# Optimization experiments

Hardware: AMD Instinct MI355X
Metric: run time of the kernel (lower is better)

Reference implementation:

```python
import jax, jax.numpy as jnp
import numpy as np

HIDDEN = 512
BATCH = 32
SEQ = 4096


def setup_inputs() -> dict:
    key = jax.random.key(0)
    ks = jax.random.split(key, 8)
    s = 1.0 / np.sqrt(HIDDEN)
    return {
        "encoder_outputs": jax.random.normal(ks[0], (BATCH, SEQ, HIDDEN), jnp.float32),
        "decoder_hidden": jax.random.normal(ks[1], (BATCH, HIDDEN), jnp.float32),
        "W_enc": jax.random.uniform(ks[2], (HIDDEN, HIDDEN), jnp.float32, -s, s),
        "b_enc": jax.random.uniform(ks[3], (HIDDEN,), jnp.float32, -s, s),
        "W_dec": jax.random.uniform(ks[4], (HIDDEN, HIDDEN), jnp.float32, -s, s),
        "b_dec": jax.random.uniform(ks[5], (HIDDEN,), jnp.float32, -s, s),
        "W_v": jax.random.uniform(ks[6], (HIDDEN, 1), jnp.float32, -s, s),
        "b_v": jax.random.uniform(ks[7], (1,), jnp.float32, -s, s),
    }


def reference(encoder_outputs, decoder_hidden, W_enc, b_enc, W_dec, b_dec, W_v, b_v):
    # (b, s, h) projected encoder states
    enc_proj = jnp.einsum("bsh,hk->bsk", encoder_outputs, W_enc) + b_enc
    # (b, 1, h) projected decoder state, broadcast-added over seq
    dec_proj = (decoder_hidden @ W_dec + b_dec)[:, None, :]
    # score: (b, s, 1)
    score = jnp.tanh(enc_proj + dec_proj) @ W_v + b_v
    attention_weights = jax.nn.softmax(score, axis=1)  # softmax over seq_len
    # context: (b, h) weighted sum of encoder outputs
    context = jnp.sum(attention_weights * encoder_outputs, axis=1)
    return context, jnp.squeeze(attention_weights, -1)
```

## Files before the change

### kernel.cpp

```cpp
#include <hip/hip_runtime.h>
#include <hip/hip_bf16.h>

typedef __attribute__((ext_vector_type(8))) short bf16x8;
typedef __attribute__((ext_vector_type(4))) float f32x4;

#define HID 512
#define NB 32
#define SEQL 4096
#define BM 64
#define NBLK 2048

#define WS_BP    0
#define WS_DPROJ (512*1024)
#define WS_SUM   (576*1024)

__device__ __forceinline__ short f2bf(float f) {
    unsigned u = __float_as_uint(f);
    unsigned r = (u + 0x7fffu + ((u >> 16) & 1u)) >> 16;
    return (short)r;
}

__device__ __forceinline__ float fast_tanh(float x) {
    float e = __expf(2.0f * x);
    float r = __builtin_amdgcn_rcpf(e + 1.0f);
    return 1.0f - 2.0f * r;
}

__global__ void k_pre(const float* __restrict__ We, short* __restrict__ Bp,
                      const float* __restrict__ dec, const float* __restrict__ Wd,
                      const float* __restrict__ be, const float* __restrict__ bd,
                      float* __restrict__ dproj, float* __restrict__ out,
                      float* __restrict__ sumacc) {
    const int blk = blockIdx.x, t = threadIdx.x;
    if (blk < 128) {
        int tid  = blk * 256 + t;
        int lane = tid & 63;
        int nt   = (tid >> 6) & 31;
        int kc   = tid >> 11;
        int k0   = kc * 32 + (lane >> 4) * 8;
        int n    = nt * 16 + (lane & 15);
        bf16x8 v;
#pragma unroll
        for (int j = 0; j < 8; ++j) v[j] = f2bf(We[(size_t)(k0 + j) * HID + n]);
        *(bf16x8*)&Bp[(size_t)tid * 8] = v;
    } else if (blk < 640) {
        __shared__ float red[8][33];
        int bid2 = blk - 128;
        int b  = bid2 >> 4, kg = bid2 & 15;
        int kl = t & 31,    hc = t >> 5;
        int k  = kg * 32 + kl;
        const float* dr = dec + (size_t)b * HID;
        float a = 0.f;
#pragma unroll 8
        for (int j = 0; j < 64; ++j) {
            int h = hc * 64 + j;
            a += dr[h] * Wd[(size_t)h * HID + k];
        }
        red[hc][kl] = a;
        __syncthreads();
        if (hc == 0) {
            float s = be[k] + bd[k];
#pragma unroll
            for (int c = 0; c < 8; ++c) s += red[c][kl];
            dproj[(size_t)b * HID + k] = s;
        }
    } else {
        int bz = blk - 640;
        out[bz * 256 + t] = 0.f;
        if (bz == 0 && t < NB) sumacc[t] = 0.f;
    }
}

__global__ __launch_bounds__(256, 2)
void k_main(const float* __restrict__ E, const short* __restrict__ Bp,
            const float* __restrict__ dproj, const float* __restrict__ Wv,
            float* __restrict__ out, float* __restrict__ sumacc) {
    __shared__ short As[2][BM][40];
    __shared__ float fbuf[640];
    __shared__ float pbuf[BM];

    const int tid  = threadIdx.x;
    const int wave = tid >> 6, lane = tid & 63;
    const int quad = lane >> 4, l15 = lane & 15;
    const int bid  = blockIdx.x;
    const int row0 = bid * BM;
    const int b    = bid >> 6;

    f32x4 acc[4][8];
#pragma unroll
    for (int r = 0; r < 4; ++r)
#pragma unroll
        for (int c = 0; c < 8; ++c) acc[r][c] = (f32x4){0.f, 0.f, 0.f, 0.f};

    const int arow = tid >> 2, ac8 = (tid & 3) * 8;
    const float* aptr = E + (size_t)(row0 + arow) * HID + ac8;

    const short* bpw = Bp + ((size_t)(wave * 8) * 64 + lane) * 8;

    {
        float4 a0 = *(const float4*)(aptr);
        float4 a1 = *(const float4*)(aptr + 4);
        bf16x8 av;
        av[0] = f2bf(a0.x); av[1] = f2bf(a0.y); av[2] = f2bf(a0.z); av[3] = f2bf(a0.w);
        av[4] = f2bf(a1.x); av[5] = f2bf(a1.y); av[6] = f2bf(a1.z); av[7] = f2bf(a1.w);
        *(bf16x8*)&As[0][arow][ac8] = av;
        __syncthreads();
    }

    for (int kc = 0; kc < 16; ++kc) {
        const int cur = kc & 1, nxt = cur ^ 1;
        float4 a0, a1;
        if (kc < 15) {
            a0 = *(const float4*)(aptr + (kc + 1) * 32);
            a1 = *(const float4*)(aptr + (kc + 1) * 32 + 4);
        }
        bf16x8 fa[4];
#pragma unroll
        for (int r = 0; r < 4; ++r)
            fa[r] = *(bf16x8*)&As[cur][r * 16 + l15][quad * 8];
        const short* bsrc = bpw + (size_t)kc * 16384;
        bf16x8 fb[8];
#pragma unroll
        for (int c = 0; c < 8; ++c)
            fb[c] = *(const bf16x8*)(bsrc + c * 512);
#pragma unroll
        for (int c = 0; c < 8; ++c)
#pragma unroll
            for (int r = 0; r < 4; ++r)
                acc[r][c] = __builtin_amdgcn_mfma_f32_16x16x32_bf16(fa[r], fb[c], acc[r][c], 0, 0, 0);
        if (kc < 15) {
            bf16x8 av;
            av[0] = f2bf(a0.x); av[1] = f2bf(a0.y); av[2] = f2bf(a0.z); av[3] = f2bf(a0.w);
            av[4] = f2bf(a1.x); av[5] = f2bf(a1.y); av[6] = f2bf(a1.z); av[7] = f2bf(a1.w);
            *(bf16x8*)&As[nxt][arow][ac8] = av;
        }
        __syncthreads();
    }

    float part[4][4];
#pragma unroll
    for (int r = 0; r < 4; ++r)
#pragma unroll
        for (int g = 0; g < 4; ++g) part[r][g] = 0.f;
    const float* dp = dproj + (size_t)b * HID;
#pragma unroll
    for (int c = 0; c < 8; ++c) {
        int col = wave * 128 + c * 16 + l15;
        float dv = dp[col];
        float wv = Wv[col];
#pragma unroll
        for (int r = 0; r < 4; ++r)
#pragma unroll
            for (int g = 0; g < 4; ++g)
                part[r][g] += fast_tanh(acc[r][c][g] + dv) * wv;
    }
#pragma unroll
    for (int r = 0; r < 4; ++r)
#pragma unroll
        for (int g = 0; g < 4; ++g) {
            float v = part[r][g];
            v += __shfl_xor(v, 1); v += __shfl_xor(v, 2);
            v += __shfl_xor(v, 4); v += __shfl_xor(v, 8);
            part[r][g] = v;
        }
    if (l15 == 0) {
#pragma unroll
        for (int r = 0; r < 4; ++r)
#pragma unroll
            for (int g = 0; g < 4; ++g)
                fbuf[wave * 64 + r * 16 + quad * 4 + g] = part[r][g];
    }
    __syncthreads();
    if (tid < 64) {
        float s  = fbuf[tid] + fbuf[64 + tid] + fbuf[128 + tid] + fbuf[192 + tid];
        float pv = __expf(s);
        pbuf[tid] = pv;
        out[(size_t)NB * HID + row0 + tid] = pv;
        float t2 = pv;
        t2 += __shfl_xor(t2, 1);  t2 += __shfl_xor(t2, 2);  t2 += __shfl_xor(t2, 4);
        t2 += __shfl_xor(t2, 8);  t2 += __shfl_xor(t2, 16); t2 += __shfl_xor(t2, 32);
        if (tid == 0) atomicAdd(&sumacc[b], t2);
    }
    __syncthreads();

    const int hq = tid & 127, rh = tid >> 7;
    const float4* E4 = (const float4*)E;
    size_t cbase = (size_t)(row0 + rh * 32) * (HID / 4) + hq;
    float4 ca = {0.f, 0.f, 0.f, 0.f};
#pragma unroll 4
    for (int rr = 0; rr < 32; ++rr) {
        float w  = pbuf[rh * 32 + rr];
        float4 e = E4[cbase + (size_t)rr * (HID / 4)];
        ca.x += w * e.x; ca.y += w * e.y; ca.z += w * e.z; ca.w += w * e.w;
    }
    if (rh == 1) {
        fbuf[hq] = ca.x; fbuf[128 + hq] = ca.y; fbuf[256 + hq] = ca.z; fbuf[384 + hq] = ca.w;
    }
    __syncthreads();
    if (rh == 0) {
        ca.x += fbuf[hq]; ca.y += fbuf[128 + hq]; ca.z += fbuf[256 + hq]; ca.w += fbuf[384 + hq];
        float* cg = out + (size_t)b * HID + hq * 4;
        atomicAdd(cg + 0, ca.x); atomicAdd(cg + 1, ca.y);
        atomicAdd(cg + 2, ca.z); atomicAdd(cg + 3, ca.w);
    }
}

__global__ void k_finish(float* __restrict__ out, const float* __restrict__ sumacc) {
    int idx = blockIdx.x * 256 + threadIdx.x;
    if (idx < NB * HID) {
        out[idx] *= 1.0f / sumacc[idx >> 9];
    } else {
        int w = idx - NB * HID;
        out[idx] *= 1.0f / sumacc[w >> 12];
    }
}

extern "C" void kernel_launch(void* const* d_in, const int* in_sizes, int n_in,
                              void* d_out, int out_size, void* d_ws, size_t ws_size,
                              hipStream_t stream) {
    const float* E   = (const float*)d_in[0];
    const float* dec = (const float*)d_in[1];
    const float* We  = (const float*)d_in[2];
    const float* be  = (const float*)d_in[3];
    const float* Wd  = (const float*)d_in[4];
    const float* bd  = (const float*)d_in[5];
    const float* Wv  = (const float*)d_in[6];
    float* out = (float*)d_out;
    char*  ws  = (char*)d_ws;
    short* Bp     = (short*)(ws + WS_BP);
    float* dproj  = (float*)(ws + WS_DPROJ);
    float* sumacc = (float*)(ws + WS_SUM);

    k_pre<<<704, 256, 0, stream>>>(We, Bp, dec, Wd, be, bd, dproj, out, sumacc);
    k_main<<<NBLK, 256, 0, stream>>>(E, Bp, dproj, Wv, out, sumacc);
    k_finish<<<576, 256, 0, stream>>>(out, sumacc);
}
```

Measured before the change: 513.1 us.

## Drop LDS staging for A, halve row tile, stagger K start per block

Each wave now loads its A fragments straight from global memory into registers and converts them with packed bf16 conversion instructions, so the LDS double buffer and the per-iteration barriers are gone. The row tile shrinks from 64 to 32 so the grid doubles, and occupancy is raised to 3 blocks per SIMD. The K-chunk start is rotated per block to spread contention on the shared B matrix. In exchange every wave re-reads the same A rows from global memory (redundant loads across the four waves), the launch count doubles, and there are twice as many context atomics.

```diff
diff --git a/kernel.cpp b/kernel.cpp
--- a/kernel.cpp
+++ b/kernel.cpp
@@ -7,8 +7,8 @@
 #define HID 512
 #define NB 32
 #define SEQL 4096
-#define BM 64
-#define NBLK 2048
+#define BM 32
+#define NBLK 4096
 
 #define WS_BP    0
 #define WS_DPROJ (512*1024)
@@ -24,6 +24,18 @@
     float e = __expf(2.0f * x);
     float r = __builtin_amdgcn_rcpf(e + 1.0f);
     return 1.0f - 2.0f * r;
+}
+
+__device__ __forceinline__ unsigned cvtpk(float lo, float hi) {
+    unsigned r;
+    asm("v_cvt_pk_bf16_f32 %0, %1, %2" : "=v"(r) : "v"(lo), "v"(hi));
+    return r;
+}
+__device__ __forceinline__ bf16x8 pack8(const float4& A, const float4& B) {
+    union { unsigned u[4]; bf16x8 v; } t;
+    t.u[0] = cvtpk(A.x, A.y); t.u[1] = cvtpk(A.z, A.w);
+    t.u[2] = cvtpk(B.x, B.y); t.u[3] = cvtpk(B.z, B.w);
+    return t.v;
 }
 
 __global__ void k_pre(const float* __restrict__ We, short* __restrict__ Bp,
@@ -71,12 +83,11 @@
     }
 }
 
-__global__ __launch_bounds__(256, 2)
+__global__ __launch_bounds__(256, 3)
 void k_main(const float* __restrict__ E, const short* __restrict__ Bp,
             const float* __restrict__ dproj, const float* __restrict__ Wv,
             float* __restrict__ out, float* __restrict__ sumacc) {
-    __shared__ short As[2][BM][40];
-    __shared__ float fbuf[640];
+    __shared__ float fbuf[512];
     __shared__ float pbuf[BM];
 
     const int tid  = threadIdx.x;
@@ -84,62 +95,53 @@
     const int quad = lane >> 4, l15 = lane & 15;
     const int bid  = blockIdx.x;
     const int row0 = bid * BM;
-    const int b    = bid >> 6;
-
-    f32x4 acc[4][8];
-#pragma unroll
-    for (int r = 0; r < 4; ++r)
+    const int b    = bid >> 7;
+    const int stag = bid & 15;
+
+    f32x4 acc[2][8];
+#pragma unroll
+    for (int r = 0; r < 2; ++r)
 #pragma unroll
         for (int c = 0; c < 8; ++c) acc[r][c] = (f32x4){0.f, 0.f, 0.f, 0.f};
 
-    const int arow = tid >> 2, ac8 = (tid & 3) * 8;
-    const float* aptr = E + (size_t)(row0 + arow) * HID + ac8;
-
+    const float* a0p = E + (size_t)(row0 + l15) * HID + quad * 8;
+    const float* a1p = E + (size_t)(row0 + 16 + l15) * HID + quad * 8;
     const short* bpw = Bp + ((size_t)(wave * 8) * 64 + lane) * 8;
 
-    {
-        float4 a0 = *(const float4*)(aptr);
-        float4 a1 = *(const float4*)(aptr + 4);
-        bf16x8 av;
-        av[0] = f2bf(a0.x); av[1] = f2bf(a0.y); av[2] = f2bf(a0.z); av[3] = f2bf(a0.w);
-        av[4] = f2bf(a1.x); av[5] = f2bf(a1.y); av[6] = f2bf(a1.z); av[7] = f2bf(a1.w);
-        *(bf16x8*)&As[0][arow][ac8] = av;
-        __syncthreads();
-    }
+    int kcs = stag;
+    float4 a00 = *(const float4*)(a0p + kcs * 32);
+    float4 a01 = *(const float4*)(a0p + kcs * 32 + 4);
+    float4 a10 = *(const float4*)(a1p + kcs * 32);
+    float4 a11 = *(const float4*)(a1p + kcs * 32 + 4);
 
     for (int kc = 0; kc < 16; ++kc) {
-        const int cur = kc & 1, nxt = cur ^ 1;
-        float4 a0, a1;
-        if (kc < 15) {
-            a0 = *(const float4*)(aptr + (kc + 1) * 32);
-            a1 = *(const float4*)(aptr + (kc + 1) * 32 + 4);
-        }
-        bf16x8 fa[4];
-#pragma unroll
-        for (int r = 0; r < 4; ++r)
-            fa[r] = *(bf16x8*)&As[cur][r * 16 + l15][quad * 8];
-        const short* bsrc = bpw + (size_t)kc * 16384;
+        const short* bsrc = bpw + (size_t)kcs * 16384;
         bf16x8 fb[8];
 #pragma unroll
         for (int c = 0; c < 8; ++c)
             fb[c] = *(const bf16x8*)(bsrc + c * 512);
-#pragma unroll
-        for (int c = 0; c < 8; ++c)
-#pragma unroll
-            for (int r = 0; r < 4; ++r)
-                acc[r][c] = __builtin_amdgcn_mfma_f32_16x16x32_bf16(fa[r], fb[c], acc[r][c], 0, 0, 0);
+        const int kn = (kcs + 1) & 15;
+        float4 n00, n01, n10, n11;
         if (kc < 15) {
-            bf16x8 av;
-            av[0] = f2bf(a0.x); av[1] = f2bf(a0.y); av[2] = f2bf(a0.z); av[3] = f2bf(a0.w);
-            av[4] = f2bf(a1.x); av[5] = f2bf(a1.y); av[6] = f2bf(a1.z); av[7] = f2bf(a1.w);
-            *(bf16x8*)&As[nxt][arow][ac8] = av;
-        }
-        __syncthreads();
-    }
-
-    float part[4][4];
-#pragma unroll
-    for (int r = 0; r < 4; ++r)
+            n00 = *(const float4*)(a0p + kn * 32);
+            n01 = *(const float4*)(a0p + kn * 32 + 4);
+            n10 = *(const float4*)(a1p + kn * 32);
+            n11 = *(const float4*)(a1p + kn * 32 + 4);
+        }
+        bf16x8 fa0 = pack8(a00, a01);
+        bf16x8 fa1 = pack8(a10, a11);
+#pragma unroll
+        for (int c = 0; c < 8; ++c) {
+            acc[0][c] = __builtin_amdgcn_mfma_f32_16x16x32_bf16(fa0, fb[c], acc[0][c], 0, 0, 0);
+            acc[1][c] = __builtin_amdgcn_mfma_f32_16x16x32_bf16(fa1, fb[c], acc[1][c], 0, 0, 0);
+        }
+        if (kc < 15) { a00 = n00; a01 = n01; a10 = n10; a11 = n11; }
+        kcs = kn;
+    }
+
+    float part[2][4];
+#pragma unroll
+    for (int r = 0; r < 2; ++r)
 #pragma unroll
         for (int g = 0; g < 4; ++g) part[r][g] = 0.f;
     const float* dp = dproj + (size_t)b * HID;
@@ -149,13 +151,13 @@
         float dv = dp[col];
         float wv = Wv[col];
 #pragma unroll
-        for (int r = 0; r < 4; ++r)
+        for (int r = 0; r < 2; ++r)
 #pragma unroll
             for (int g = 0; g < 4; ++g)
                 part[r][g] += fast_tanh(acc[r][c][g] + dv) * wv;
     }
 #pragma unroll
-    for (int r = 0; r < 4; ++r)
+    for (int r = 0; r < 2; ++r)
 #pragma unroll
         for (int g = 0; g < 4; ++g) {
             float v = part[r][g];
@@ -165,31 +167,31 @@
         }
     if (l15 == 0) {
 #pragma unroll
-        for (int r = 0; r < 4; ++r)
+        for (int r = 0; r < 2; ++r)
 #pragma unroll
             for (int g = 0; g < 4; ++g)
-                fbuf[wave * 64 + r * 16 + quad * 4 + g] = part[r][g];
+                fbuf[wave * 32 + r * 16 + quad * 4 + g] = part[r][g];
     }
     __syncthreads();
-    if (tid < 64) {
-        float s  = fbuf[tid] + fbuf[64 + tid] + fbuf[128 + tid] + fbuf[192 + tid];
+    if (tid < 32) {
+        float s  = fbuf[tid] + fbuf[32 + tid] + fbuf[64 + tid] + fbuf[96 + tid];
         float pv = __expf(s);
         pbuf[tid] = pv;
         out[(size_t)NB * HID + row0 + tid] = pv;
         float t2 = pv;
-        t2 += __shfl_xor(t2, 1);  t2 += __shfl_xor(t2, 2);  t2 += __shfl_xor(t2, 4);
-        t2 += __shfl_xor(t2, 8);  t2 += __shfl_xor(t2, 16); t2 += __shfl_xor(t2, 32);
+        t2 += __shfl_xor(t2, 1); t2 += __shfl_xor(t2, 2); t2 += __shfl_xor(t2, 4);
+        t2 += __shfl_xor(t2, 8); t2 += __shfl_xor(t2, 16);
         if (tid == 0) atomicAdd(&sumacc[b], t2);
     }
     __syncthreads();
 
     const int hq = tid & 127, rh = tid >> 7;
     const float4* E4 = (const float4*)E;
-    size_t cbase = (size_t)(row0 + rh * 32) * (HID / 4) + hq;
+    size_t cbase = (size_t)(row0 + rh * 16) * (HID / 4) + hq;
     float4 ca = {0.f, 0.f, 0.f, 0.f};
 #pragma unroll 4
-    for (int rr = 0; rr < 32; ++rr) {
-        float w  = pbuf[rh * 32 + rr];
+    for (int rr = 0; rr < 16; ++rr) {
+        float w  = pbuf[rh * 16 + rr];
         float4 e = E4[cbase + (size_t)rr * (HID / 4)];
         ca.x += w * e.x; ca.y += w * e.y; ca.z += w * e.z; ca.w += w * e.w;
     }
```

Result: slower. 544.1 us (+6.0%).

## Stage whole A tile in LDS upfront and double-buffer B fragments in registers

Applied to the files above, without the earlier changes.

Each block now loads its full 64x512 encoder tile once, converts it to bf16 with packed cvt instructions, and stores it in LDS. This removes the per-k-chunk syncthreads and global A loads. B fragments are prefetched one k-chunk ahead into registers, and blocks start at different k offsets to spread L2 traffic on the shared weight matrix. In exchange, LDS use per block rises to about 66KB and register pressure grows from the double-buffered B fragments and the full unroll, which may cut occupancy.

```diff
diff --git a/kernel.cpp b/kernel.cpp
--- a/kernel.cpp
+++ b/kernel.cpp
@@ -3,6 +3,7 @@
 
 typedef __attribute__((ext_vector_type(8))) short bf16x8;
 typedef __attribute__((ext_vector_type(4))) float f32x4;
+typedef __attribute__((ext_vector_type(4))) short s16x4;
 
 #define HID 512
 #define NB 32
@@ -24,6 +25,12 @@
     float e = __expf(2.0f * x);
     float r = __builtin_amdgcn_rcpf(e + 1.0f);
     return 1.0f - 2.0f * r;
+}
+
+__device__ __forceinline__ unsigned cvtpk(float lo, float hi) {
+    unsigned r;
+    asm("v_cvt_pk_bf16_f32 %0, %1, %2" : "=v"(r) : "v"(lo), "v"(hi));
+    return r;
 }
 
 __global__ void k_pre(const float* __restrict__ We, short* __restrict__ Bp,
@@ -75,7 +82,7 @@
 void k_main(const float* __restrict__ E, const short* __restrict__ Bp,
             const float* __restrict__ dproj, const float* __restrict__ Wv,
             float* __restrict__ out, float* __restrict__ sumacc) {
-    __shared__ short As[2][BM][40];
+    __shared__ short As[BM][520];
     __shared__ float fbuf[640];
     __shared__ float pbuf[BM];
 
@@ -85,6 +92,23 @@
     const int bid  = blockIdx.x;
     const int row0 = bid * BM;
     const int b    = bid >> 6;
+    const int stag = bid & 15;
+
+    {
+        const float4* src4 = (const float4*)(E + (size_t)(row0 + wave * 16) * HID);
+#pragma unroll
+        for (int i = 0; i < 32; ++i) {
+            float4 v = src4[i * 64 + lane];
+            int fo  = i * 256 + lane * 4;
+            int r16 = fo >> 9;
+            int col = fo & 511;
+            union { unsigned u[2]; s16x4 s; } t;
+            t.u[0] = cvtpk(v.x, v.y);
+            t.u[1] = cvtpk(v.z, v.w);
+            *(s16x4*)&As[wave * 16 + r16][col] = t.s;
+        }
+    }
+    __syncthreads();
 
     f32x4 acc[4][8];
 #pragma unroll
@@ -92,50 +116,33 @@
 #pragma unroll
         for (int c = 0; c < 8; ++c) acc[r][c] = (f32x4){0.f, 0.f, 0.f, 0.f};
 
-    const int arow = tid >> 2, ac8 = (tid & 3) * 8;
-    const float* aptr = E + (size_t)(row0 + arow) * HID + ac8;
-
     const short* bpw = Bp + ((size_t)(wave * 8) * 64 + lane) * 8;
 
-    {
-        float4 a0 = *(const float4*)(aptr);
-        float4 a1 = *(const float4*)(aptr + 4);
-        bf16x8 av;
-        av[0] = f2bf(a0.x); av[1] = f2bf(a0.y); av[2] = f2bf(a0.z); av[3] = f2bf(a0.w);
-        av[4] = f2bf(a1.x); av[5] = f2bf(a1.y); av[6] = f2bf(a1.z); av[7] = f2bf(a1.w);
-        *(bf16x8*)&As[0][arow][ac8] = av;
-        __syncthreads();
-    }
-
+#define LOADB(dst, kk) do {                                            \
+        const short* bsrc_ = bpw + (size_t)(kk) * 16384;               \
+        _Pragma("unroll")                                              \
+        for (int c_ = 0; c_ < 8; ++c_)                                 \
+            dst[c_] = *(const bf16x8*)(bsrc_ + c_ * 512);              \
+    } while (0)
+
+    bf16x8 fb[2][8];
+    LOADB(fb[0], stag);
+#pragma unroll
     for (int kc = 0; kc < 16; ++kc) {
         const int cur = kc & 1, nxt = cur ^ 1;
-        float4 a0, a1;
-        if (kc < 15) {
-            a0 = *(const float4*)(aptr + (kc + 1) * 32);
-            a1 = *(const float4*)(aptr + (kc + 1) * 32 + 4);
-        }
+        const int kcs = (stag + kc) & 15;
+        if (kc < 15) LOADB(fb[nxt], (kcs + 1) & 15);
         bf16x8 fa[4];
 #pragma unroll
         for (int r = 0; r < 4; ++r)
-            fa[r] = *(bf16x8*)&As[cur][r * 16 + l15][quad * 8];
-        const short* bsrc = bpw + (size_t)kc * 16384;
-        bf16x8 fb[8];
+            fa[r] = *(bf16x8*)&As[r * 16 + l15][kcs * 32 + quad * 8];
 #pragma unroll
         for (int c = 0; c < 8; ++c)
-            fb[c] = *(const bf16x8*)(bsrc + c * 512);
-#pragma unroll
-        for (int c = 0; c < 8; ++c)
 #pragma unroll
             for (int r = 0; r < 4; ++r)
-                acc[r][c] = __builtin_amdgcn_mfma_f32_16x16x32_bf16(fa[r], fb[c], acc[r][c], 0, 0, 0);
-        if (kc < 15) {
-            bf16x8 av;
-            av[0] = f2bf(a0.x); av[1] = f2bf(a0.y); av[2] = f2bf(a0.z); av[3] = f2bf(a0.w);
-            av[4] = f2bf(a1.x); av[5] = f2bf(a1.y); av[6] = f2bf(a1.z); av[7] = f2bf(a1.w);
-            *(bf16x8*)&As[nxt][arow][ac8] = av;
-        }
-        __syncthreads();
-    }
+                acc[r][c] = __builtin_amdgcn_mfma_f32_16x16x32_bf16(fa[r], fb[cur][c], acc[r][c], 0, 0, 0);
+    }
+#undef LOADB
 
     float part[4][4];
 #pragma unroll
```

Result: faster. 460.6 us (-10.2%).
